# Performance work log

Measured on AMD Instinct MI355X. Metric: run time of the kernel, lower is better.

Reference implementation:

```python
import jax, jax.numpy as jnp
import numpy as np

L, D, H = 2, 1024, 1024  # num_layers, input_size, hidden_size
S, B = 512, 32           # seq_len, batch


def setup_inputs() -> dict:
    key = jax.random.key(0)
    ks = jax.random.split(key, 12)
    k = 1.0 / H
    lim = np.sqrt(k).astype(np.float32)
    u = lambda kk, shape: jax.random.uniform(kk, shape, jnp.float32, -lim, lim)
    return {
        "x": jax.random.normal(ks[0], (S, B, D), jnp.float32),
        "h0": jax.random.normal(ks[1], (L, B, H), jnp.float32),
        "Wz": u(ks[2], (L, H, D)), "Wr": u(ks[3], (L, H, D)), "Wh": u(ks[4], (L, H, D)),
        "Uz": u(ks[5], (L, H, H)), "Ur": u(ks[6], (L, H, H)), "Uh": u(ks[7], (L, H, H)),
        "bz": u(ks[8], (L, H)), "br": u(ks[9], (L, H)), "bh": u(ks[10], (L, H)),
    }


def _gru_forward(x, h0, Wz, Wr, Wh, Uz, Ur, Uh, bz, br, bh):
    # NOTE: in this module every layer consumes the ORIGINAL x[t] (not the
    # previous layer's output), so layers are independent recurrences and can
    # be vectorized over the layer axis; scan handles the sequential time axis.
    # Precompute input projections for all steps/layers: [S, L, B, H]
    xz = jnp.einsum('sbd,lhd->slbh', x, Wz) + bz[None, :, None, :]
    xr = jnp.einsum('sbd,lhd->slbh', x, Wr) + br[None, :, None, :]
    xh = jnp.einsum('sbd,lhd->slbh', x, Wh) + bh[None, :, None, :]

    def step(h, xs):  # h: [L,B,H]
        xz_t, xr_t, xh_t = xs
        z = jax.nn.sigmoid(xz_t + jnp.einsum('lbh,lgh->lbg', h, Uz))
        r = jax.nn.sigmoid(xr_t + jnp.einsum('lbh,lgh->lbg', h, Ur))
        hh = jnp.tanh(xh_t + jnp.einsum('lbh,lgh->lbg', r * h, Uh))
        h_new = (1.0 - z) * h + z * hh
        return h_new, h_new[-1]

    h_n, output = jax.lax.scan(step, h0, (xz, xr, xh))
    return output, h_n  # [S,B,H], [L,B,H]


def reference(x, h0, Wz, Wr, Wh, Uz, Ur, Uh, bz, br, bh):
    return _gru_forward(x, h0, Wz, Wr, Wh, Uz, Ur, Uh, bz, br, bh)
```

## Files before the change

kernel.cpp:

```cpp
#include <hip/hip_runtime.h>
#include <stdint.h>


typedef __attribute__((ext_vector_type(8))) short bf16x8;
typedef __attribute__((ext_vector_type(4))) float f32x4;
typedef __attribute__((ext_vector_type(4))) unsigned int u32x4;

#define NL 2
#define SB 32
#define HD 1024
#define SEQ 512

#define XG_ELEMS   ((size_t)SEQ*6*SB*HD)
#define XG_OFF     0ull
#define XBF_OFF    (XG_OFF + XG_ELEMS*2)
#define XBF_ELEMS  ((size_t)SEQ*SB*HD)
#define WBF_OFF    (XBF_OFF + XBF_ELEMS*2)
#define WBF_ELEMS  ((size_t)6*HD*HD)
#define HBUF_OFF   (WBF_OFF + WBF_ELEMS*2)
#define HBUF_BYTES ((size_t)NL*SB*HD*2)
#define RBUF_OFF   (HBUF_OFF + HBUF_BYTES)
#define HFLG_OFF   (RBUF_OFF + HBUF_BYTES)
#define FLG_WORDS  (4*64*16)
#define RFLG_OFF   (HFLG_OFF + FLG_WORDS*4)
#define WS_NEED    (RFLG_OFF + FLG_WORDS*4)

__device__ __forceinline__ unsigned short f2bf(float f) {
  unsigned int u = __float_as_uint(f);
  u = u + 0x7fffu + ((u >> 16) & 1u);
  return (unsigned short)(u >> 16);
}
__device__ __forceinline__ float bf2f(unsigned int bits) {
  return __uint_as_float(bits << 16);
}
__device__ __forceinline__ f32x4 unpack4(uint2 u) {
  f32x4 v;
  v[0] = bf2f(u.x & 0xffffu); v[1] = bf2f(u.x >> 16);
  v[2] = bf2f(u.y & 0xffffu); v[3] = bf2f(u.y >> 16);
  return v;
}

__device__ __forceinline__ void st_wt(unsigned long long* p, unsigned long long v) {
  __hip_atomic_store(p, v, __ATOMIC_RELAXED, __HIP_MEMORY_SCOPE_AGENT);
}
__device__ __forceinline__ unsigned ld_flag(const unsigned* p) {
  return __hip_atomic_load(p, __ATOMIC_RELAXED, __HIP_MEMORY_SCOPE_AGENT);
}
__device__ __forceinline__ void st_flag(unsigned* p, unsigned v) {
  __hip_atomic_store(p, v, __ATOMIC_RELAXED, __HIP_MEMORY_SCOPE_AGENT);
}

__global__ void cvt_f32_bf16(const float* __restrict__ src,
                             unsigned short* __restrict__ dst, int n4) {
  int i = blockIdx.x * blockDim.x + threadIdx.x;
  int st = gridDim.x * blockDim.x;
  for (; i < n4; i += st) {
    float4 v = ((const float4*)src)[i];
    ushort4 o = { f2bf(v.x), f2bf(v.y), f2bf(v.z), f2bf(v.w) };
    ((ushort4*)dst)[i] = o;
  }
}

__global__ __launch_bounds__(256) void gemm_xg(const unsigned short* __restrict__ Wb,
                                               const unsigned short* __restrict__ xb,
                                               unsigned short* __restrict__ xg) {
  __shared__ short As[128 * 32];
  __shared__ short Bs[128 * 32];
  const int lg = blockIdx.z;
  const int m0 = blockIdx.y * 128;
  const int n0 = blockIdx.x * 128;
  const int tid = threadIdx.x, w = tid >> 6, lane = tid & 63;
  const int wm = (w >> 1) * 64, wn = (w & 1) * 64;
  const unsigned short* Ag = Wb + (size_t)lg * HD * HD;

  f32x4 acc[4][4] = {};

  for (int k0 = 0; k0 < HD; k0 += 32) {
    __syncthreads();
#pragma unroll
    for (int i = 0; i < 2; i++) {
      int off = (i * 256 + tid) * 16;
      int rr = off >> 6;
      int cc = (off >> 4) & 3;
      *(uint4*)((char*)As + off) = *(const uint4*)(Ag + (size_t)(m0 + rr) * HD + k0 + cc * 8);
      *(uint4*)((char*)Bs + off) = *(const uint4*)(xb + (size_t)(n0 + rr) * HD + k0 + cc * 8);
    }
    __syncthreads();
    bf16x8 af[4], bf[4];
#pragma unroll
    for (int mi = 0; mi < 4; mi++)
      af[mi] = *(const bf16x8*)&As[(wm + mi * 16 + (lane & 15)) * 32 + ((lane >> 4) << 3)];
#pragma unroll
    for (int ni = 0; ni < 4; ni++)
      bf[ni] = *(const bf16x8*)&Bs[(wn + ni * 16 + (lane & 15)) * 32 + ((lane >> 4) << 3)];
#pragma unroll
    for (int mi = 0; mi < 4; mi++)
#pragma unroll
      for (int ni = 0; ni < 4; ni++)
        acc[mi][ni] = __builtin_amdgcn_mfma_f32_16x16x32_bf16(af[mi], bf[ni], acc[mi][ni], 0, 0, 0);
  }

#pragma unroll
  for (int mi = 0; mi < 4; mi++) {
    int g = m0 + wm + mi * 16 + ((lane >> 4) << 2);
#pragma unroll
    for (int ni = 0; ni < 4; ni++) {
      int n = n0 + wn + ni * 16 + (lane & 15);
      int s = n >> 5, b = n & 31;
      ushort4 o = { f2bf(acc[mi][ni][0]), f2bf(acc[mi][ni][1]),
                    f2bf(acc[mi][ni][2]), f2bf(acc[mi][ni][3]) };
      *(ushort4*)(xg + ((size_t)(s * 6 + lg)) * (SB * HD) + (size_t)b * HD + g) = o;
    }
  }
}

__device__ __forceinline__ bf16x8 afrag(const short* wlds, int gate, int lane, int k) {
  int r = lane & 15;
  int kk = k + ((lane >> 4) << 3);
  int ck = (kk >> 3) ^ (r & 7);
  return *(const bf16x8*)&wlds[gate * 16384 + r * HD + (ck << 3)];
}

__device__ __forceinline__ void publish(unsigned long long* dst, const f32x4 vals,
                                        unsigned* flagword, unsigned tag, int lane) {
  ushort4 o = { f2bf(vals[0]), f2bf(vals[1]), f2bf(vals[2]), f2bf(vals[3]) };
  unsigned long long q; __builtin_memcpy(&q, &o, 8);
  st_wt(dst, q);
  asm volatile("s_waitcnt vmcnt(0)" ::: "memory");
  if (lane == 0) st_flag(flagword, tag);
}

__device__ __forceinline__ void flag_wait64(const unsigned* fgrp, int lane, unsigned tag) {
  bool ok;
  do { ok = (ld_flag(&fgrp[lane * 16]) >= tag); } while (!__all(ok));
}

__device__ __forceinline__ void stage_wide(const unsigned long long* p, u32x4* vv) {
#pragma unroll
  for (int kk = 0; kk < 32; kk++) {
    asm volatile("global_load_dwordx4 %0, %1, off sc0 sc1"
                 : "=v"(vv[kk]) : "v"(p + kk * 8) : "memory");
  }
  asm volatile("s_waitcnt vmcnt(0)" ::: "memory");
  __builtin_amdgcn_sched_barrier(0);
}

__global__ __launch_bounds__(64, 1) void gru_rec(
    const float* __restrict__ h0,
    const float* __restrict__ Uz, const float* __restrict__ Ur, const float* __restrict__ Uh,
    const float* __restrict__ bz, const float* __restrict__ br, const float* __restrict__ bh,
    const unsigned short* __restrict__ xg,
    unsigned long long* __restrict__ hbuf,
    unsigned long long* __restrict__ rbuf,
    unsigned* __restrict__ hflg,
    unsigned* __restrict__ rflg,
    float* __restrict__ out) {
  __shared__ short wlds[3 * 16 * HD];

  const int wg = blockIdx.x;
  const int l = wg >> 7;
  const int gs = wg & 63;
  const int g0 = gs * 16;
  const int b0 = ((wg >> 6) & 1) * 16;
  const int grp = wg >> 6;
  const int lane = threadIdx.x;
  const int col = lane & 15;
  const int sub = lane >> 4;
  const int rb = sub << 2;

  unsigned* hf_g = hflg + grp * 64 * 16;
  unsigned* rf_g = rflg + grp * 64 * 16;

  const float* Us[3] = { Uz, Ur, Uh };
#pragma unroll
  for (int gate = 0; gate < 3; gate++) {
    const float* U = Us[gate] + (size_t)l * HD * HD + (size_t)g0 * HD;
    for (int it = 0; it < 32; it++) {
      int chunk = it * 64 + lane;
      int r = chunk >> 7;
      int ck = chunk & 127;
      const float* src = U + (size_t)r * HD + ck * 8;
      float4 a = *(const float4*)src;
      float4 bq = *(const float4*)(src + 4);
      bf16x8 o;
      o[0] = (short)f2bf(a.x); o[1] = (short)f2bf(a.y);
      o[2] = (short)f2bf(a.z); o[3] = (short)f2bf(a.w);
      o[4] = (short)f2bf(bq.x); o[5] = (short)f2bf(bq.y);
      o[6] = (short)f2bf(bq.z); o[7] = (short)f2bf(bq.w);
      int sck = ck ^ (r & 7);
      *(bf16x8*)&wlds[gate * 16384 + r * HD + sck * 8] = o;
    }
  }
  asm volatile("s_waitcnt lgkmcnt(0)" ::: "memory");

  f32x4 vbz = *(const f32x4*)(bz + l * HD + g0 + rb);
  f32x4 vbr = *(const f32x4*)(br + l * HD + g0 + rb);
  f32x4 vbh = *(const f32x4*)(bh + l * HD + g0 + rb);

  const int brow = l * SB + b0 + col;
  f32x4 hreg = *(const f32x4*)(h0 + (size_t)brow * HD + g0 + rb);

  unsigned long long* hdst = hbuf + ((size_t)brow << 8) + ((g0 + rb) >> 2);
  unsigned long long* rdst = rbuf + ((size_t)brow << 8) + ((g0 + rb) >> 2);
  const unsigned long long* hp = hbuf + ((size_t)brow << 8) + sub * 2;
  const unsigned long long* rp = rbuf + ((size_t)brow << 8) + sub * 2;

  publish(hdst, hreg, &hf_g[gs * 16], 1u, lane);

  size_t xb0 = ((size_t)l * 3) * (SB * HD) + (size_t)(b0 + col) * HD + g0 + rb;
  uint2 xzc = *(const uint2*)(xg + xb0);
  uint2 xrc = *(const uint2*)(xg + xb0 + SB * HD);
  uint2 xhc = *(const uint2*)(xg + xb0 + 2 * SB * HD);
  uint2 xzn, xrn, xhn;

  u32x4 vv[32];

  for (int s = 0; s < SEQ; s++) {
    const unsigned tag = (unsigned)(s + 1);

    flag_wait64(hf_g, lane, tag);
    stage_wide(hp, vv);
    f32x4 az0 = {0,0,0,0}, az1 = {0,0,0,0}, ar0 = {0,0,0,0}, ar1 = {0,0,0,0};
#pragma unroll
    for (int kk = 0; kk < 32; kk++) {
      union { u32x4 w; bf16x8 b; } u;
      u.w = vv[kk];
      bf16x8 wz = afrag(wlds, 0, lane, kk * 32);
      bf16x8 wr = afrag(wlds, 1, lane, kk * 32);
      if (kk & 1) {
        az1 = __builtin_amdgcn_mfma_f32_16x16x32_bf16(wz, u.b, az1, 0, 0, 0);
        ar1 = __builtin_amdgcn_mfma_f32_16x16x32_bf16(wr, u.b, ar1, 0, 0, 0);
      } else {
        az0 = __builtin_amdgcn_mfma_f32_16x16x32_bf16(wz, u.b, az0, 0, 0, 0);
        ar0 = __builtin_amdgcn_mfma_f32_16x16x32_bf16(wr, u.b, ar0, 0, 0, 0);
      }
    }
    f32x4 accz = az0 + az1, accr = ar0 + ar1;
    f32x4 xzf = unpack4(xzc), xrf = unpack4(xrc);
    f32x4 z, rh;
#pragma unroll
    for (int j = 0; j < 4; j++) {
      float za = xzf[j] + vbz[j] + accz[j];
      float ra = xrf[j] + vbr[j] + accr[j];
      z[j] = 1.f / (1.f + __expf(-za));
      rh[j] = (1.f / (1.f + __expf(-ra))) * hreg[j];
    }
    publish(rdst, rh, &rf_g[gs * 16], tag, lane);

    {
      int sn = (s + 1 < SEQ) ? s + 1 : s;
      size_t xbn = ((size_t)sn * 6 + l * 3) * (SB * HD) + (size_t)(b0 + col) * HD + g0 + rb;
      xzn = *(const uint2*)(xg + xbn);
      xrn = *(const uint2*)(xg + xbn + SB * HD);
      xhn = *(const uint2*)(xg + xbn + 2 * SB * HD);
    }

    flag_wait64(rf_g, lane, tag);
    stage_wide(rp, vv);
    f32x4 ah0 = {0,0,0,0}, ah1 = {0,0,0,0};
#pragma unroll
    for (int kk = 0; kk < 32; kk++) {
      union { u32x4 w; bf16x8 b; } u;
      u.w = vv[kk];
      bf16x8 wh = afrag(wlds, 2, lane, kk * 32);
      if (kk & 1) ah1 = __builtin_amdgcn_mfma_f32_16x16x32_bf16(wh, u.b, ah1, 0, 0, 0);
      else        ah0 = __builtin_amdgcn_mfma_f32_16x16x32_bf16(wh, u.b, ah0, 0, 0, 0);
    }
    f32x4 acch = ah0 + ah1;
    f32x4 xhf = unpack4(xhc);
#pragma unroll
    for (int j = 0; j < 4; j++) {
      float ha = xhf[j] + vbh[j] + acch[j];
      float e = __expf(2.f * ha);
      float hh = 1.f - 2.f / (e + 1.f);
      hreg[j] = (1.f - z[j]) * hreg[j] + z[j] * hh;
    }
    publish(hdst, hreg, &hf_g[gs * 16], tag + 1, lane);

    if (l == 1)
      *(f32x4*)(out + (size_t)s * (SB * HD) + (size_t)(b0 + col) * HD + g0 + rb) = hreg;
    if (s == SEQ - 1)
      *(f32x4*)(out + (size_t)SEQ * SB * HD + (size_t)brow * HD + g0 + rb) = hreg;

    xzc = xzn; xrc = xrn; xhc = xhn;
  }
}

extern "C" void kernel_launch(void* const* d_in, const int* in_sizes, int n_in,
                              void* d_out, int out_size, void* d_ws, size_t ws_size,
                              hipStream_t stream) {
  const float* x  = (const float*)d_in[0];
  const float* h0 = (const float*)d_in[1];
  const float* Wz = (const float*)d_in[2];
  const float* Wr = (const float*)d_in[3];
  const float* Wh = (const float*)d_in[4];
  const float* Uz = (const float*)d_in[5];
  const float* Ur = (const float*)d_in[6];
  const float* Uh = (const float*)d_in[7];
  const float* bz = (const float*)d_in[8];
  const float* br = (const float*)d_in[9];
  const float* bh = (const float*)d_in[10];

  char* ws = (char*)d_ws;
  unsigned short* xg  = (unsigned short*)(ws + XG_OFF);
  unsigned short* xbf = (unsigned short*)(ws + XBF_OFF);
  unsigned short* wbf = (unsigned short*)(ws + WBF_OFF);

  hipMemsetAsync(ws + HFLG_OFF, 0, FLG_WORDS * 8, stream);

  cvt_f32_bf16<<<1024, 256, 0, stream>>>(x, xbf, (int)(XBF_ELEMS / 4));
  const float* Wsrc[3] = { Wz, Wr, Wh };
  for (int gate = 0; gate < 3; gate++)
    for (int l = 0; l < 2; l++)
      cvt_f32_bf16<<<512, 256, 0, stream>>>(Wsrc[gate] + (size_t)l * HD * HD,
                                            wbf + ((size_t)(l * 3 + gate)) * HD * HD,
                                            HD * HD / 4);

  gemm_xg<<<dim3(128, 8, 6), 256, 0, stream>>>(wbf, xbf, xg);

  gru_rec<<<256, 64, 0, stream>>>(h0, Uz, Ur, Uh, bz, br, bh, xg,
                                  (unsigned long long*)(ws + HBUF_OFF),
                                  (unsigned long long*)(ws + RBUF_OFF),
                                  (unsigned*)(ws + HFLG_OFF),
                                  (unsigned*)(ws + RFLG_OFF),
                                  (float*)d_out);
}
```

Baseline: 4.372 ms.

## Replicate hidden-state buffers and flags to spread polling contention across copies

Each workgroup now writes its h and r*h slices and their ready flags into eight replicated buffers, and each reader polls and loads from the copy picked by its slice index. The goal is to spread the many concurrent flag polls and wide loads of the same cache lines across different addresses, cutting hot-spot contention in the cross-workgroup exchange every step. In exchange every publish issues eight times as many stores and flag writes on the critical path, and the flag area to memset grows.

```diff
diff --git a/kernel.cpp b/kernel.cpp
--- a/kernel.cpp
+++ b/kernel.cpp
@@ -10,6 +10,7 @@
 #define SB 32
 #define HD 1024
 #define SEQ 512
+#define NREP 8
 
 #define XG_ELEMS   ((size_t)SEQ*6*SB*HD)
 #define XG_OFF     0ull
@@ -17,13 +18,14 @@
 #define XBF_ELEMS  ((size_t)SEQ*SB*HD)
 #define WBF_OFF    (XBF_OFF + XBF_ELEMS*2)
 #define WBF_ELEMS  ((size_t)6*HD*HD)
+#define REP_U64S   ((size_t)NL*SB*256)
 #define HBUF_OFF   (WBF_OFF + WBF_ELEMS*2)
-#define HBUF_BYTES ((size_t)NL*SB*HD*2)
-#define RBUF_OFF   (HBUF_OFF + HBUF_BYTES)
-#define HFLG_OFF   (RBUF_OFF + HBUF_BYTES)
-#define FLG_WORDS  (4*64*16)
-#define RFLG_OFF   (HFLG_OFF + FLG_WORDS*4)
-#define WS_NEED    (RFLG_OFF + FLG_WORDS*4)
+#define RBUF_OFF   (HBUF_OFF + REP_U64S*NREP*8)
+#define FLG_WORDS_REP (4*64*16)
+#define HFLG_OFF   (RBUF_OFF + REP_U64S*NREP*8)
+#define RFLG_OFF   (HFLG_OFF + (size_t)FLG_WORDS_REP*NREP*4)
+#define FLG_BYTES  ((size_t)FLG_WORDS_REP*NREP*4)
+#define WS_NEED    (RFLG_OFF + FLG_BYTES)
 
 __device__ __forceinline__ unsigned short f2bf(float f) {
   unsigned int u = __float_as_uint(f);
@@ -121,13 +123,19 @@
   return *(const bf16x8*)&wlds[gate * 16384 + r * HD + (ck << 3)];
 }
 
-__device__ __forceinline__ void publish(unsigned long long* dst, const f32x4 vals,
-                                        unsigned* flagword, unsigned tag, int lane) {
+__device__ __forceinline__ void publish(unsigned long long* dst0, const f32x4 vals,
+                                        unsigned* flag0, unsigned tag, int lane) {
   ushort4 o = { f2bf(vals[0]), f2bf(vals[1]), f2bf(vals[2]), f2bf(vals[3]) };
   unsigned long long q; __builtin_memcpy(&q, &o, 8);
-  st_wt(dst, q);
+#pragma unroll
+  for (int rep = 0; rep < NREP; rep++)
+    st_wt(dst0 + (size_t)rep * REP_U64S, q);
   asm volatile("s_waitcnt vmcnt(0)" ::: "memory");
-  if (lane == 0) st_flag(flagword, tag);
+  if (lane == 0) {
+#pragma unroll
+    for (int rep = 0; rep < NREP; rep++)
+      st_flag(flag0 + (size_t)rep * FLG_WORDS_REP, tag);
+  }
 }
 
 __device__ __forceinline__ void flag_wait64(const unsigned* fgrp, int lane, unsigned tag) {
@@ -167,9 +175,7 @@
   const int col = lane & 15;
   const int sub = lane >> 4;
   const int rb = sub << 2;
-
-  unsigned* hf_g = hflg + grp * 64 * 16;
-  unsigned* rf_g = rflg + grp * 64 * 16;
+  const int rep = gs & 7;
 
   const float* Us[3] = { Uz, Ur, Uh };
 #pragma unroll
@@ -202,10 +208,14 @@
 
   unsigned long long* hdst = hbuf + ((size_t)brow << 8) + ((g0 + rb) >> 2);
   unsigned long long* rdst = rbuf + ((size_t)brow << 8) + ((g0 + rb) >> 2);
-  const unsigned long long* hp = hbuf + ((size_t)brow << 8) + sub * 2;
-  const unsigned long long* rp = rbuf + ((size_t)brow << 8) + sub * 2;
-
-  publish(hdst, hreg, &hf_g[gs * 16], 1u, lane);
+  unsigned* hflag0 = hflg + (grp * 64 + gs) * 16;
+  unsigned* rflag0 = rflg + (grp * 64 + gs) * 16;
+  const unsigned long long* hp = hbuf + (size_t)rep * REP_U64S + ((size_t)brow << 8) + sub * 2;
+  const unsigned long long* rp = rbuf + (size_t)rep * REP_U64S + ((size_t)brow << 8) + sub * 2;
+  const unsigned* hf_g = hflg + (size_t)rep * FLG_WORDS_REP + grp * 64 * 16;
+  const unsigned* rf_g = rflg + (size_t)rep * FLG_WORDS_REP + grp * 64 * 16;
+
+  publish(hdst, hreg, hflag0, 1u, lane);
 
   size_t xb0 = ((size_t)l * 3) * (SB * HD) + (size_t)(b0 + col) * HD + g0 + rb;
   uint2 xzc = *(const uint2*)(xg + xb0);
@@ -245,7 +255,7 @@
       z[j] = 1.f / (1.f + __expf(-za));
       rh[j] = (1.f / (1.f + __expf(-ra))) * hreg[j];
     }
-    publish(rdst, rh, &rf_g[gs * 16], tag, lane);
+    publish(rdst, rh, rflag0, tag, lane);
 
     {
       int sn = (s + 1 < SEQ) ? s + 1 : s;
@@ -275,7 +285,7 @@
       float hh = 1.f - 2.f / (e + 1.f);
       hreg[j] = (1.f - z[j]) * hreg[j] + z[j] * hh;
     }
-    publish(hdst, hreg, &hf_g[gs * 16], tag + 1, lane);
+    publish(hdst, hreg, hflag0, tag + 1, lane);
 
     if (l == 1)
       *(f32x4*)(out + (size_t)s * (SB * HD) + (size_t)(b0 + col) * HD + g0 + rb) = hreg;
@@ -306,7 +316,7 @@
   unsigned short* xbf = (unsigned short*)(ws + XBF_OFF);
   unsigned short* wbf = (unsigned short*)(ws + WBF_OFF);
 
-  hipMemsetAsync(ws + HFLG_OFF, 0, FLG_WORDS * 8, stream);
+  hipMemsetAsync(ws + HFLG_OFF, 0, FLG_BYTES * 2, stream);
 
   cvt_f32_bf16<<<1024, 256, 0, stream>>>(x, xbf, (int)(XBF_ELEMS / 4));
   const float* Wsrc[3] = { Wz, Wr, Wh };
```

After: 4.618 ms. +5.6%, slower.

## Split recurrent GEMV over K halves with pairwise partial-sum exchange

Applied to the files above, without the earlier changes.

Each workgroup now owns 32 gate rows but only half of the K dimension (512), and exchanges bf16 partial sums with its paired workgroup through global memory plus a per-pair flag before applying the gate nonlinearities. This halves the per-step hidden-state staging and the MFMA chain length per workgroup, shortening the serial critical path of each timestep. In exchange it adds two extra global round-trips with flag spin-waits per step, and partial sums are rounded to bf16, which slightly changes numerics.

```diff
diff --git a/kernel.cpp b/kernel.cpp
--- a/kernel.cpp
+++ b/kernel.cpp
@@ -18,12 +18,17 @@
 #define WBF_OFF    (XBF_OFF + XBF_ELEMS*2)
 #define WBF_ELEMS  ((size_t)6*HD*HD)
 #define HBUF_OFF   (WBF_OFF + WBF_ELEMS*2)
-#define HBUF_BYTES ((size_t)NL*SB*HD*2)
+#define HBUF_BYTES ((size_t)NL*SB*256*8)
 #define RBUF_OFF   (HBUF_OFF + HBUF_BYTES)
 #define HFLG_OFF   (RBUF_OFF + HBUF_BYTES)
 #define FLG_WORDS  (4*64*16)
 #define RFLG_OFF   (HFLG_OFF + FLG_WORDS*4)
-#define WS_NEED    (RFLG_OFF + FLG_WORDS*4)
+#define PAF_OFF    (RFLG_OFF + FLG_WORDS*4)
+#define PBF_OFF    (PAF_OFF + 256*16*4)
+#define CLR_BYTES  ((PBF_OFF + 256*16*4) - HFLG_OFF)
+#define PA_OFF     (PBF_OFF + 256*16*4)
+#define PB_OFF     (PA_OFF + (size_t)256*256*8)
+#define WS_NEED    (PB_OFF + (size_t)256*128*8)
 
 __device__ __forceinline__ unsigned short f2bf(float f) {
   unsigned int u = __float_as_uint(f);
@@ -39,15 +44,27 @@
   v[2] = bf2f(u.y & 0xffffu); v[3] = bf2f(u.y >> 16);
   return v;
 }
+__device__ __forceinline__ f32x4 unpack4q(unsigned long long q) {
+  uint2 u = { (unsigned)q, (unsigned)(q >> 32) };
+  return unpack4(u);
+}
 
 __device__ __forceinline__ void st_wt(unsigned long long* p, unsigned long long v) {
   __hip_atomic_store(p, v, __ATOMIC_RELAXED, __HIP_MEMORY_SCOPE_AGENT);
 }
+__device__ __forceinline__ unsigned long long ld_wt(const unsigned long long* p) {
+  return __hip_atomic_load(p, __ATOMIC_RELAXED, __HIP_MEMORY_SCOPE_AGENT);
+}
 __device__ __forceinline__ unsigned ld_flag(const unsigned* p) {
   return __hip_atomic_load(p, __ATOMIC_RELAXED, __HIP_MEMORY_SCOPE_AGENT);
 }
 __device__ __forceinline__ void st_flag(unsigned* p, unsigned v) {
   __hip_atomic_store(p, v, __ATOMIC_RELAXED, __HIP_MEMORY_SCOPE_AGENT);
+}
+__device__ __forceinline__ unsigned long long pack4(const f32x4 v) {
+  ushort4 o = { f2bf(v[0]), f2bf(v[1]), f2bf(v[2]), f2bf(v[3]) };
+  unsigned long long q; __builtin_memcpy(&q, &o, 8);
+  return q;
 }
 
 __global__ void cvt_f32_bf16(const float* __restrict__ src,
@@ -114,30 +131,24 @@
   }
 }
 
-__device__ __forceinline__ bf16x8 afrag(const short* wlds, int gate, int lane, int k) {
-  int r = lane & 15;
-  int kk = k + ((lane >> 4) << 3);
-  int ck = (kk >> 3) ^ (r & 7);
-  return *(const bf16x8*)&wlds[gate * 16384 + r * HD + (ck << 3)];
-}
-
-__device__ __forceinline__ void publish(unsigned long long* dst, const f32x4 vals,
-                                        unsigned* flagword, unsigned tag, int lane) {
-  ushort4 o = { f2bf(vals[0]), f2bf(vals[1]), f2bf(vals[2]), f2bf(vals[3]) };
-  unsigned long long q; __builtin_memcpy(&q, &o, 8);
-  st_wt(dst, q);
-  asm volatile("s_waitcnt vmcnt(0)" ::: "memory");
-  if (lane == 0) st_flag(flagword, tag);
+__device__ __forceinline__ bf16x8 afrag2(const short* wlds, int gate, int rt,
+                                         int lane, int kk) {
+  int r = rt * 16 + (lane & 15);
+  int sck = (kk * 4 + (lane >> 4)) ^ (r & 7);
+  return *(const bf16x8*)&wlds[gate * 16384 + r * 512 + sck * 8];
 }
 
 __device__ __forceinline__ void flag_wait64(const unsigned* fgrp, int lane, unsigned tag) {
   bool ok;
   do { ok = (ld_flag(&fgrp[lane * 16]) >= tag); } while (!__all(ok));
 }
-
-__device__ __forceinline__ void stage_wide(const unsigned long long* p, u32x4* vv) {
-#pragma unroll
-  for (int kk = 0; kk < 32; kk++) {
+__device__ __forceinline__ void flag_wait1(const unsigned* f, unsigned tag) {
+  while (ld_flag(f) < tag) {}
+}
+
+__device__ __forceinline__ void stage16(const unsigned long long* p, u32x4* vv) {
+#pragma unroll
+  for (int kk = 0; kk < 16; kk++) {
     asm volatile("global_load_dwordx4 %0, %1, off sc0 sc1"
                  : "=v"(vv[kk]) : "v"(p + kk * 8) : "memory");
   }
@@ -154,31 +165,36 @@
     unsigned long long* __restrict__ rbuf,
     unsigned* __restrict__ hflg,
     unsigned* __restrict__ rflg,
+    unsigned long long* __restrict__ pa,
+    unsigned long long* __restrict__ pb,
+    unsigned* __restrict__ paf,
+    unsigned* __restrict__ pbf,
     float* __restrict__ out) {
-  __shared__ short wlds[3 * 16 * HD];
+  __shared__ short wlds[3 * 16384];
 
   const int wg = blockIdx.x;
   const int l = wg >> 7;
-  const int gs = wg & 63;
-  const int g0 = gs * 16;
-  const int b0 = ((wg >> 6) & 1) * 16;
-  const int grp = wg >> 6;
+  const int r7 = wg & 127;
+  const int kh = r7 >> 6;
+  const int bhalf = (r7 >> 5) & 1;
+  const int gs = r7 & 31;
+  const int g0 = gs * 32;
   const int lane = threadIdx.x;
   const int col = lane & 15;
   const int sub = lane >> 4;
   const int rb = sub << 2;
-
-  unsigned* hf_g = hflg + grp * 64 * 16;
-  unsigned* rf_g = rflg + grp * 64 * 16;
+  const int grp = l * 2 + bhalf;
+  const int pid = gs * 2 + kh;
+  const int pidx = ((l * 32 + gs) * 2 + bhalf) * 2 + kh;
 
   const float* Us[3] = { Uz, Ur, Uh };
 #pragma unroll
   for (int gate = 0; gate < 3; gate++) {
-    const float* U = Us[gate] + (size_t)l * HD * HD + (size_t)g0 * HD;
+    const float* U = Us[gate] + (size_t)l * HD * HD + (size_t)g0 * HD + kh * 512;
     for (int it = 0; it < 32; it++) {
       int chunk = it * 64 + lane;
-      int r = chunk >> 7;
-      int ck = chunk & 127;
+      int r = chunk >> 6;
+      int ck = chunk & 63;
       const float* src = U + (size_t)r * HD + ck * 8;
       float4 a = *(const float4*)src;
       float4 bq = *(const float4*)(src + 4);
@@ -188,101 +204,162 @@
       o[4] = (short)f2bf(bq.x); o[5] = (short)f2bf(bq.y);
       o[6] = (short)f2bf(bq.z); o[7] = (short)f2bf(bq.w);
       int sck = ck ^ (r & 7);
-      *(bf16x8*)&wlds[gate * 16384 + r * HD + sck * 8] = o;
+      *(bf16x8*)&wlds[gate * 16384 + r * 512 + sck * 8] = o;
     }
   }
   asm volatile("s_waitcnt lgkmcnt(0)" ::: "memory");
 
-  f32x4 vbz = *(const f32x4*)(bz + l * HD + g0 + rb);
-  f32x4 vbr = *(const f32x4*)(br + l * HD + g0 + rb);
-  f32x4 vbh = *(const f32x4*)(bh + l * HD + g0 + rb);
-
-  const int brow = l * SB + b0 + col;
-  f32x4 hreg = *(const f32x4*)(h0 + (size_t)brow * HD + g0 + rb);
-
-  unsigned long long* hdst = hbuf + ((size_t)brow << 8) + ((g0 + rb) >> 2);
-  unsigned long long* rdst = rbuf + ((size_t)brow << 8) + ((g0 + rb) >> 2);
-  const unsigned long long* hp = hbuf + ((size_t)brow << 8) + sub * 2;
-  const unsigned long long* rp = rbuf + ((size_t)brow << 8) + sub * 2;
-
-  publish(hdst, hreg, &hf_g[gs * 16], 1u, lane);
-
-  size_t xb0 = ((size_t)l * 3) * (SB * HD) + (size_t)(b0 + col) * HD + g0 + rb;
-  uint2 xzc = *(const uint2*)(xg + xb0);
-  uint2 xrc = *(const uint2*)(xg + xb0 + SB * HD);
-  uint2 xhc = *(const uint2*)(xg + xb0 + 2 * SB * HD);
-  uint2 xzn, xrn, xhn;
-
-  u32x4 vv[32];
+  f32x4 vbz[2], vbr[2], vbh[2];
+#pragma unroll
+  for (int rt = 0; rt < 2; rt++) {
+    vbz[rt] = *(const f32x4*)(bz + l * HD + g0 + rt * 16 + rb);
+    vbr[rt] = *(const f32x4*)(br + l * HD + g0 + rt * 16 + rb);
+    vbh[rt] = *(const f32x4*)(bh + l * HD + g0 + rt * 16 + rb);
+  }
+
+  const int brow = l * SB + bhalf * 16 + col;
+  f32x4 hreg[2];
+#pragma unroll
+  for (int rt = 0; rt < 2; rt++)
+    hreg[rt] = *(const f32x4*)(h0 + (size_t)brow * HD + g0 + rt * 16 + rb);
+
+  unsigned long long* hdst = hbuf + ((size_t)brow << 8) + ((g0 + kh * 16 + rb) >> 2);
+  unsigned long long* rdst = rbuf + ((size_t)brow << 8) + ((g0 + kh * 16 + rb) >> 2);
+  const unsigned long long* hp = hbuf + ((size_t)brow << 8) + kh * 128 + sub * 2;
+  const unsigned long long* rp = rbuf + ((size_t)brow << 8) + kh * 128 + sub * 2;
+  const unsigned* hf_g = hflg + grp * 64 * 16;
+  const unsigned* rf_g = rflg + grp * 64 * 16;
+  unsigned* myhf = hflg + (grp * 64 + pid) * 16;
+  unsigned* myrf = rflg + (grp * 64 + pid) * 16;
+
+  unsigned long long* paw = pa + (size_t)pidx * 256;
+  const unsigned long long* par = pa + (size_t)(pidx ^ 1) * 256;
+  unsigned long long* pbw = pb + (size_t)pidx * 128;
+  const unsigned long long* pbr = pb + (size_t)(pidx ^ 1) * 128;
+  unsigned* pafw = paf + pidx * 16;
+  const unsigned* pafr = paf + (pidx ^ 1) * 16;
+  unsigned* pbfw = pbf + pidx * 16;
+  const unsigned* pbfr = pbf + (pidx ^ 1) * 16;
+
+  st_wt(hdst, pack4(hreg[kh]));
+  asm volatile("s_waitcnt vmcnt(0)" ::: "memory");
+  if (lane == 0) st_flag(myhf, 1u);
+
+  uint2 xc[3][2], xn[3][2];
+  {
+    size_t xb0 = ((size_t)l * 3) * (SB * HD) + (size_t)(bhalf * 16 + col) * HD + g0 + rb;
+#pragma unroll
+    for (int g3 = 0; g3 < 3; g3++)
+#pragma unroll
+      for (int rt = 0; rt < 2; rt++)
+        xc[g3][rt] = *(const uint2*)(xg + xb0 + g3 * (SB * HD) + rt * 16);
+  }
+
+  u32x4 vv[16];
 
   for (int s = 0; s < SEQ; s++) {
     const unsigned tag = (unsigned)(s + 1);
 
     flag_wait64(hf_g, lane, tag);
-    stage_wide(hp, vv);
-    f32x4 az0 = {0,0,0,0}, az1 = {0,0,0,0}, ar0 = {0,0,0,0}, ar1 = {0,0,0,0};
-#pragma unroll
-    for (int kk = 0; kk < 32; kk++) {
+    stage16(hp, vv);
+    f32x4 az[2] = { {0,0,0,0}, {0,0,0,0} }, ar[2] = { {0,0,0,0}, {0,0,0,0} };
+#pragma unroll
+    for (int kk = 0; kk < 16; kk++) {
       union { u32x4 w; bf16x8 b; } u;
       u.w = vv[kk];
-      bf16x8 wz = afrag(wlds, 0, lane, kk * 32);
-      bf16x8 wr = afrag(wlds, 1, lane, kk * 32);
-      if (kk & 1) {
-        az1 = __builtin_amdgcn_mfma_f32_16x16x32_bf16(wz, u.b, az1, 0, 0, 0);
-        ar1 = __builtin_amdgcn_mfma_f32_16x16x32_bf16(wr, u.b, ar1, 0, 0, 0);
-      } else {
-        az0 = __builtin_amdgcn_mfma_f32_16x16x32_bf16(wz, u.b, az0, 0, 0, 0);
-        ar0 = __builtin_amdgcn_mfma_f32_16x16x32_bf16(wr, u.b, ar0, 0, 0, 0);
+#pragma unroll
+      for (int rt = 0; rt < 2; rt++) {
+        az[rt] = __builtin_amdgcn_mfma_f32_16x16x32_bf16(afrag2(wlds, 0, rt, lane, kk), u.b, az[rt], 0, 0, 0);
+        ar[rt] = __builtin_amdgcn_mfma_f32_16x16x32_bf16(afrag2(wlds, 1, rt, lane, kk), u.b, ar[rt], 0, 0, 0);
       }
     }
-    f32x4 accz = az0 + az1, accr = ar0 + ar1;
-    f32x4 xzf = unpack4(xzc), xrf = unpack4(xrc);
-    f32x4 z, rh;
-#pragma unroll
-    for (int j = 0; j < 4; j++) {
-      float za = xzf[j] + vbz[j] + accz[j];
-      float ra = xrf[j] + vbr[j] + accr[j];
-      z[j] = 1.f / (1.f + __expf(-za));
-      rh[j] = (1.f / (1.f + __expf(-ra))) * hreg[j];
-    }
-    publish(rdst, rh, &rf_g[gs * 16], tag, lane);
+#pragma unroll
+    for (int rt = 0; rt < 2; rt++) {
+      st_wt(paw + (0 * 16 + col) * 8 + rt * 4 + sub, pack4(az[rt]));
+      st_wt(paw + (1 * 16 + col) * 8 + rt * 4 + sub, pack4(ar[rt]));
+    }
+    asm volatile("s_waitcnt vmcnt(0)" ::: "memory");
+    if (lane == 0) st_flag(pafw, tag);
+    flag_wait1(pafr, tag);
+    f32x4 pz[2], pr[2];
+#pragma unroll
+    for (int rt = 0; rt < 2; rt++) {
+      pz[rt] = unpack4q(ld_wt(par + (0 * 16 + col) * 8 + rt * 4 + sub));
+      pr[rt] = unpack4q(ld_wt(par + (1 * 16 + col) * 8 + rt * 4 + sub));
+    }
+    f32x4 z[2], rh[2];
+#pragma unroll
+    for (int rt = 0; rt < 2; rt++) {
+      f32x4 xzf = unpack4(xc[0][rt]), xrf = unpack4(xc[1][rt]);
+#pragma unroll
+      for (int j = 0; j < 4; j++) {
+        float za = xzf[j] + vbz[rt][j] + az[rt][j] + pz[rt][j];
+        float ra = xrf[j] + vbr[rt][j] + ar[rt][j] + pr[rt][j];
+        z[rt][j] = 1.f / (1.f + __expf(-za));
+        rh[rt][j] = (1.f / (1.f + __expf(-ra))) * hreg[rt][j];
+      }
+    }
+    st_wt(rdst, pack4(rh[kh]));
+    asm volatile("s_waitcnt vmcnt(0)" ::: "memory");
+    if (lane == 0) st_flag(myrf, tag);
 
     {
       int sn = (s + 1 < SEQ) ? s + 1 : s;
-      size_t xbn = ((size_t)sn * 6 + l * 3) * (SB * HD) + (size_t)(b0 + col) * HD + g0 + rb;
-      xzn = *(const uint2*)(xg + xbn);
-      xrn = *(const uint2*)(xg + xbn + SB * HD);
-      xhn = *(const uint2*)(xg + xbn + 2 * SB * HD);
+      size_t xbn = ((size_t)sn * 6 + l * 3) * (SB * HD) + (size_t)(bhalf * 16 + col) * HD + g0 + rb;
+#pragma unroll
+      for (int g3 = 0; g3 < 3; g3++)
+#pragma unroll
+        for (int rt = 0; rt < 2; rt++)
+          xn[g3][rt] = *(const uint2*)(xg + xbn + g3 * (SB * HD) + rt * 16);
     }
 
     flag_wait64(rf_g, lane, tag);
-    stage_wide(rp, vv);
-    f32x4 ah0 = {0,0,0,0}, ah1 = {0,0,0,0};
-#pragma unroll
-    for (int kk = 0; kk < 32; kk++) {
+    stage16(rp, vv);
+    f32x4 ah[2] = { {0,0,0,0}, {0,0,0,0} };
+#pragma unroll
+    for (int kk = 0; kk < 16; kk++) {
       union { u32x4 w; bf16x8 b; } u;
       u.w = vv[kk];
-      bf16x8 wh = afrag(wlds, 2, lane, kk * 32);
-      if (kk & 1) ah1 = __builtin_amdgcn_mfma_f32_16x16x32_bf16(wh, u.b, ah1, 0, 0, 0);
-      else        ah0 = __builtin_amdgcn_mfma_f32_16x16x32_bf16(wh, u.b, ah0, 0, 0, 0);
-    }
-    f32x4 acch = ah0 + ah1;
-    f32x4 xhf = unpack4(xhc);
-#pragma unroll
-    for (int j = 0; j < 4; j++) {
-      float ha = xhf[j] + vbh[j] + acch[j];
-      float e = __expf(2.f * ha);
-      float hh = 1.f - 2.f / (e + 1.f);
-      hreg[j] = (1.f - z[j]) * hreg[j] + z[j] * hh;
-    }
-    publish(hdst, hreg, &hf_g[gs * 16], tag + 1, lane);
+#pragma unroll
+      for (int rt = 0; rt < 2; rt++)
+        ah[rt] = __builtin_amdgcn_mfma_f32_16x16x32_bf16(afrag2(wlds, 2, rt, lane, kk), u.b, ah[rt], 0, 0, 0);
+    }
+#pragma unroll
+    for (int rt = 0; rt < 2; rt++)
+      st_wt(pbw + col * 8 + rt * 4 + sub, pack4(ah[rt]));
+    asm volatile("s_waitcnt vmcnt(0)" ::: "memory");
+    if (lane == 0) st_flag(pbfw, tag);
+    flag_wait1(pbfr, tag);
+    f32x4 ph[2];
+#pragma unroll
+    for (int rt = 0; rt < 2; rt++)
+      ph[rt] = unpack4q(ld_wt(pbr + col * 8 + rt * 4 + sub));
+
+#pragma unroll
+    for (int rt = 0; rt < 2; rt++) {
+      f32x4 xhf = unpack4(xc[2][rt]);
+#pragma unroll
+      for (int j = 0; j < 4; j++) {
+        float ha = xhf[j] + vbh[rt][j] + ah[rt][j] + ph[rt][j];
+        float e = __expf(2.f * ha);
+        float hh = 1.f - 2.f / (e + 1.f);
+        hreg[rt][j] = (1.f - z[rt][j]) * hreg[rt][j] + z[rt][j] * hh;
+      }
+    }
+    st_wt(hdst, pack4(hreg[kh]));
+    asm volatile("s_waitcnt vmcnt(0)" ::: "memory");
+    if (lane == 0) st_flag(myhf, tag + 1);
 
     if (l == 1)
-      *(f32x4*)(out + (size_t)s * (SB * HD) + (size_t)(b0 + col) * HD + g0 + rb) = hreg;
+      *(f32x4*)(out + (size_t)s * (SB * HD) + (size_t)(bhalf * 16 + col) * HD + g0 + kh * 16 + rb) = hreg[kh];
     if (s == SEQ - 1)
-      *(f32x4*)(out + (size_t)SEQ * SB * HD + (size_t)brow * HD + g0 + rb) = hreg;
-
-    xzc = xzn; xrc = xrn; xhc = xhn;
+      *(f32x4*)(out + (size_t)SEQ * SB * HD + (size_t)brow * HD + g0 + kh * 16 + rb) = hreg[kh];
+
+#pragma unroll
+    for (int g3 = 0; g3 < 3; g3++)
+#pragma unroll
+      for (int rt = 0; rt < 2; rt++)
+        xc[g3][rt] = xn[g3][rt];
   }
 }
 
@@ -306,7 +383,7 @@
   unsigned short* xbf = (unsigned short*)(ws + XBF_OFF);
   unsigned short* wbf = (unsigned short*)(ws + WBF_OFF);
 
-  hipMemsetAsync(ws + HFLG_OFF, 0, FLG_WORDS * 8, stream);
+  hipMemsetAsync(ws + HFLG_OFF, 0, CLR_BYTES, stream);
 
   cvt_f32_bf16<<<1024, 256, 0, stream>>>(x, xbf, (int)(XBF_ELEMS / 4));
   const float* Wsrc[3] = { Wz, Wr, Wh };
@@ -323,5 +400,9 @@
                                   (unsigned long long*)(ws + RBUF_OFF),
                                   (unsigned*)(ws + HFLG_OFF),
                                   (unsigned*)(ws + RFLG_OFF),
+                                  (unsigned long long*)(ws + PA_OFF),
+                                  (unsigned long long*)(ws + PB_OFF),
+                                  (unsigned*)(ws + PAF_OFF),
+                                  (unsigned*)(ws + PBF_OFF),
                                   (float*)d_out);
 }
```

Measured after the change: 5.157 ms. 1.18x slower.

## Reorder GRU step to publish r gate early and overlap z gate compute

Applied to the files above, without the earlier changes.

The recurrent step now computes the reset-gate matvec first and publishes r*h before the update-gate matvec. The z-gate MFMAs then run while other workgroups fill the r buffer, which takes them off the critical path between the h and r flag waits. Each wide staging load is also split: the first half of the MFMAs starts once 16 of the 32 loads land (vmcnt(16)), overlapping load latency with compute. This depends on loads completing in order and keeps the staged h vector live longer.

```diff
diff --git a/kernel.cpp b/kernel.cpp
--- a/kernel.cpp
+++ b/kernel.cpp
@@ -135,12 +135,18 @@
   do { ok = (ld_flag(&fgrp[lane * 16]) >= tag); } while (!__all(ok));
 }
 
-__device__ __forceinline__ void stage_wide(const unsigned long long* p, u32x4* vv) {
+__device__ __forceinline__ void stage_issue(const unsigned long long* p, u32x4* vv) {
 #pragma unroll
   for (int kk = 0; kk < 32; kk++) {
     asm volatile("global_load_dwordx4 %0, %1, off sc0 sc1"
                  : "=v"(vv[kk]) : "v"(p + kk * 8) : "memory");
   }
+}
+__device__ __forceinline__ void wait_16() {
+  asm volatile("s_waitcnt vmcnt(16)" ::: "memory");
+  __builtin_amdgcn_sched_barrier(0);
+}
+__device__ __forceinline__ void wait_0() {
   asm volatile("s_waitcnt vmcnt(0)" ::: "memory");
   __builtin_amdgcn_sched_barrier(0);
 }
@@ -219,30 +225,32 @@
     const unsigned tag = (unsigned)(s + 1);
 
     flag_wait64(hf_g, lane, tag);
-    stage_wide(hp, vv);
-    f32x4 az0 = {0,0,0,0}, az1 = {0,0,0,0}, ar0 = {0,0,0,0}, ar1 = {0,0,0,0};
-#pragma unroll
-    for (int kk = 0; kk < 32; kk++) {
-      union { u32x4 w; bf16x8 b; } u;
-      u.w = vv[kk];
-      bf16x8 wz = afrag(wlds, 0, lane, kk * 32);
+    stage_issue(hp, vv);
+    f32x4 ar0 = {0,0,0,0}, ar1 = {0,0,0,0};
+    wait_16();
+#pragma unroll
+    for (int kk = 0; kk < 16; kk++) {
+      union { u32x4 w; bf16x8 b; } u;
+      u.w = vv[kk];
       bf16x8 wr = afrag(wlds, 1, lane, kk * 32);
-      if (kk & 1) {
-        az1 = __builtin_amdgcn_mfma_f32_16x16x32_bf16(wz, u.b, az1, 0, 0, 0);
-        ar1 = __builtin_amdgcn_mfma_f32_16x16x32_bf16(wr, u.b, ar1, 0, 0, 0);
-      } else {
-        az0 = __builtin_amdgcn_mfma_f32_16x16x32_bf16(wz, u.b, az0, 0, 0, 0);
-        ar0 = __builtin_amdgcn_mfma_f32_16x16x32_bf16(wr, u.b, ar0, 0, 0, 0);
-      }
-    }
-    f32x4 accz = az0 + az1, accr = ar0 + ar1;
-    f32x4 xzf = unpack4(xzc), xrf = unpack4(xrc);
-    f32x4 z, rh;
+      if (kk & 1) ar1 = __builtin_amdgcn_mfma_f32_16x16x32_bf16(wr, u.b, ar1, 0, 0, 0);
+      else        ar0 = __builtin_amdgcn_mfma_f32_16x16x32_bf16(wr, u.b, ar0, 0, 0, 0);
+    }
+    wait_0();
+#pragma unroll
+    for (int kk = 16; kk < 32; kk++) {
+      union { u32x4 w; bf16x8 b; } u;
+      u.w = vv[kk];
+      bf16x8 wr = afrag(wlds, 1, lane, kk * 32);
+      if (kk & 1) ar1 = __builtin_amdgcn_mfma_f32_16x16x32_bf16(wr, u.b, ar1, 0, 0, 0);
+      else        ar0 = __builtin_amdgcn_mfma_f32_16x16x32_bf16(wr, u.b, ar0, 0, 0, 0);
+    }
+    f32x4 accr = ar0 + ar1;
+    f32x4 xrf = unpack4(xrc);
+    f32x4 rh;
 #pragma unroll
     for (int j = 0; j < 4; j++) {
-      float za = xzf[j] + vbz[j] + accz[j];
       float ra = xrf[j] + vbr[j] + accr[j];
-      z[j] = 1.f / (1.f + __expf(-za));
       rh[j] = (1.f / (1.f + __expf(-ra))) * hreg[j];
     }
     publish(rdst, rh, &rf_g[gs * 16], tag, lane);
@@ -255,11 +263,39 @@
       xhn = *(const uint2*)(xg + xbn + 2 * SB * HD);
     }
 
+    f32x4 az0 = {0,0,0,0}, az1 = {0,0,0,0};
+#pragma unroll
+    for (int kk = 0; kk < 32; kk++) {
+      union { u32x4 w; bf16x8 b; } u;
+      u.w = vv[kk];
+      bf16x8 wz = afrag(wlds, 0, lane, kk * 32);
+      if (kk & 1) az1 = __builtin_amdgcn_mfma_f32_16x16x32_bf16(wz, u.b, az1, 0, 0, 0);
+      else        az0 = __builtin_amdgcn_mfma_f32_16x16x32_bf16(wz, u.b, az0, 0, 0, 0);
+    }
+    f32x4 accz = az0 + az1;
+    f32x4 xzf = unpack4(xzc);
+    f32x4 z;
+#pragma unroll
+    for (int j = 0; j < 4; j++) {
+      float za = xzf[j] + vbz[j] + accz[j];
+      z[j] = 1.f / (1.f + __expf(-za));
+    }
+
     flag_wait64(rf_g, lane, tag);
-    stage_wide(rp, vv);
+    stage_issue(rp, vv);
     f32x4 ah0 = {0,0,0,0}, ah1 = {0,0,0,0};
-#pragma unroll
-    for (int kk = 0; kk < 32; kk++) {
+    wait_16();
+#pragma unroll
+    for (int kk = 0; kk < 16; kk++) {
+      union { u32x4 w; bf16x8 b; } u;
+      u.w = vv[kk];
+      bf16x8 wh = afrag(wlds, 2, lane, kk * 32);
+      if (kk & 1) ah1 = __builtin_amdgcn_mfma_f32_16x16x32_bf16(wh, u.b, ah1, 0, 0, 0);
+      else        ah0 = __builtin_amdgcn_mfma_f32_16x16x32_bf16(wh, u.b, ah0, 0, 0, 0);
+    }
+    wait_0();
+#pragma unroll
+    for (int kk = 16; kk < 32; kk++) {
       union { u32x4 w; bf16x8 b; } u;
       u.w = vv[kk];
       bf16x8 wh = afrag(wlds, 2, lane, kk * 32);
```

New measurement: 3.821 ms. 12.6% less time.
